# Kernel optimization log

Hardware: AMD Instinct MI355X
Metric: run time of the kernel (lower is better)

## Reference

```python
import jax, jax.numpy as jnp
import numpy as np


def setup_inputs() -> dict:
    key = jax.random.key(0)
    ks = jax.random.split(key, 8)
    B, De, Do, T, H, W = 4, 128, 512, 4, 30, 52
    s = 0.05  # weight init scale
    return {
        "m_in": jax.random.normal(ks[0], (B, De, T, H, W), jnp.float32),
        "m_out": jax.random.normal(ks[1], (B, Do, T, H, W), jnp.float32),
        "q_in": jax.random.normal(ks[2], (B, De, H, W), jnp.float32),
        "q_out": jax.random.normal(ks[3], (B, Do, H, W), jnp.float32),
        "wr": jax.random.normal(ks[4], (Do, 2 * Do), jnp.float32) * s,
        "br": jnp.zeros((Do,), jnp.float32),
        "wu": jax.random.normal(ks[5], (Do, 2 * Do), jnp.float32) * s,
        "bu": jnp.zeros((Do,), jnp.float32),
        "wc": jax.random.normal(ks[6], (Do, 2 * Do), jnp.float32) * s,
        "bc": jnp.zeros((Do,), jnp.float32),
    }


def reference(m_in, m_out, q_in, q_out, wr, br, wu, bu, wc, bc):
    B, De, T, H, W = m_in.shape
    Do = m_out.shape[1]
    PROP_LAYERS = 5

    # --- memory read: pairwise frame attention (bmm + softmax + bmm) ---
    # keys: all T memory frames flattened; queries: current frame.
    mi = m_in.reshape(B, De, T * H * W)            # [B, De, THW]
    qi = q_in.reshape(B, De, H * W)                # [B, De, HW]
    p = jnp.einsum('bdk,bdq->bkq', mi, qi) / (De ** 0.5)  # [B, THW, HW]
    p = jax.nn.softmax(p, axis=1)                  # softmax over memory locations (dim=1 in torch)
    mem = jnp.einsum('bok,bkq->boq', m_out.reshape(B, Do, T * H * W), p)
    mem = mem.reshape(B, Do, H, W)                 # mem_mean; identical every propagate layer

    # --- ConvGRU_h (kernel_size=1 => per-pixel linear gates) ---
    def conv1x1(w, b, x):
        return jnp.einsum('oc,bchw->bohw', w, x) + b[None, :, None, None]

    def gru(x, h):
        xh = jnp.concatenate([x, h], axis=1)                       # [B, 2*Do, H, W]
        r = jax.nn.sigmoid(conv1x1(wr, br, xh))
        u = jax.nn.sigmoid(conv1x1(wu, bu, xh))
        c = jnp.tanh(conv1x1(wc, bc, jnp.concatenate([x, r * h], axis=1)))
        return h * (1.0 - u) + u * c

    q0 = q_out
    q = q_out
    for _ in range(PROP_LAYERS):
        q = gru(q, mem)  # original: q_out = ConvGRU_h(q_out, mem_mean)
    return jnp.concatenate([q, q0], axis=1)  # [B, 2*Do, H, W]
```

## Files before the change

### kernel.cpp

```cpp
#include <hip/hip_runtime.h>
#include <hip/hip_bf16.h>
#include <math.h>

typedef unsigned short u16;
typedef __attribute__((ext_vector_type(8))) short bf16x8;
typedef __attribute__((ext_vector_type(4))) float f32x4;

__device__ __forceinline__ u16 f2bf(float f) {
  union { float f; unsigned u; } x; x.f = f;
  unsigned r = x.u + 0x7fffu + ((x.u >> 16) & 1u);
  return (u16)(r >> 16);
}
__device__ __forceinline__ float bf2f(u16 h) {
  union { unsigned u; float f; } x; x.u = ((unsigned)h) << 16;
  return x.f;
}
__device__ __forceinline__ float sigmf(float x) {
  x = fminf(fmaxf(x, -30.f), 30.f);
  return 1.f / (1.f + __expf(-x));
}
__device__ __forceinline__ float tanh_fast(float x) {
  x = fminf(fmaxf(x, -15.f), 15.f);
  float t = __expf(2.f * x);
  return (t - 1.f) / (t + 1.f);
}

template<int N> __device__ __forceinline__ void wait_vmcnt() {
  if constexpr (N == 0)      asm volatile("s_waitcnt vmcnt(0)" ::: "memory");
  else if constexpr (N == 4) asm volatile("s_waitcnt vmcnt(4)" ::: "memory");
  else if constexpr (N == 6) asm volatile("s_waitcnt vmcnt(6)" ::: "memory");
  else if constexpr (N == 9) asm volatile("s_waitcnt vmcnt(9)" ::: "memory");
  else static_assert(N == 0 || N == 4 || N == 6 || N == 9, "add vmcnt case");
}

#define NB 4
#define DE 128
#define DO_ 512
#define HW 1560
#define THW 6240
#define NP 1664
#define KP 6272
#define PROP 5
#define PVSPLIT 7
#define PVKC 896

template<int MODE, int BMT, int BKT>
__device__ __forceinline__
void gemm_core(const u16* __restrict__ A, const u16* __restrict__ Bt,
               int K, int lda, int ldb, long a_bs, long b_bs,
               void* __restrict__ out0v, long o0_bs, int ld0,
               u16* __restrict__ out1, long o1_bs, int ld1,
               const void* __restrict__ e0v, long e0_bs,
               const void* __restrict__ e1v, long e1_bs,
               const void* __restrict__ e2v, long e2_bs,
               int nvalid, float scale)
{
  constexpr int WR = BMT / 64;
  constexpr int WC = 4 / WR;
  constexpr int NF = 8 / WC;
  constexpr int KK = BKT / 32;
  constexpr int ASLOT = BMT * BKT / 8;
  constexpr int BSLOT = 128 * BKT / 8;
  constexpr int NISS = (ASLOT + BSLOT) / 256;
  constexpr int RSH = (BMT == 128) ? 7 : 6;
  __shared__ u16 lds[2][ASLOT + BSLOT][8];

  const int tid = threadIdx.x;
  const int wave = tid >> 6, lane = tid & 63;
  const int kg = lane >> 4, lr = lane & 15;
  const int wrw = wave / WC, wcw = wave % WC;
  const long b = blockIdx.z;
  const int m0 = blockIdx.x * BMT, n0 = blockIdx.y * 128;
  A += b * a_bs; Bt += b * b_bs;

  float* out0f = (float*)out0v;
  u16* out0h = (u16*)out0v;
  const float* e0f = (const float*)e0v;
  const u16* e0h = (const u16*)e0v;
  const u16* e1h = (const u16*)e1v;
  const u16* e2h = (const u16*)e2v;

  auto stage = [&](int buf, int kt) {
#pragma unroll
    for (int i = 0; i < NISS; ++i) {
      int s = tid + 256 * i;
      const u16* src;
      if (s < ASLOT) {
        int row = s & (BMT - 1), g = s >> RSH;
        src = A + (long)(m0 + row) * lda + kt + g * 8;
      } else {
        int s2 = s - ASLOT;
        int row = s2 & 127, g = s2 >> 7;
        src = Bt + (long)(n0 + row) * ldb + kt + g * 8;
      }
      __builtin_amdgcn_global_load_lds(
          (const __attribute__((address_space(1))) void*)src,
          (__attribute__((address_space(3))) void*)&lds[buf][wave * 64 + 256 * i][0],
          16, 0, 0);
    }
  };

  f32x4 acc[4][NF];
#pragma unroll
  for (int m = 0; m < 4; ++m)
#pragma unroll
    for (int n = 0; n < NF; ++n) acc[m][n] = (f32x4){0.f, 0.f, 0.f, 0.f};

  const int nt = K / BKT;
  stage(0, 0);
  for (int t = 0; t < nt; ++t) {
    int cur = t & 1;
    if (t + 1 < nt) {
      stage(cur ^ 1, (t + 1) * BKT);
      wait_vmcnt<NISS>();
    } else {
      wait_vmcnt<0>();
    }
    __builtin_amdgcn_s_barrier();
    bf16x8 af[KK][4], bfr[KK][NF];
#pragma unroll
    for (int kk = 0; kk < KK; ++kk) {
#pragma unroll
      for (int m = 0; m < 4; ++m)
        af[kk][m] = *(const bf16x8*)&lds[cur][(kk * 4 + kg) * BMT + wrw * 64 + m * 16 + lr][0];
#pragma unroll
      for (int n = 0; n < NF; ++n)
        bfr[kk][n] = *(const bf16x8*)&lds[cur][ASLOT + (kk * 4 + kg) * 128 + (wcw * NF + n) * 16 + lr][0];
    }
#pragma unroll
    for (int kk = 0; kk < KK; ++kk)
#pragma unroll
      for (int m = 0; m < 4; ++m)
#pragma unroll
        for (int n = 0; n < NF; ++n)
          acc[m][n] = __builtin_amdgcn_mfma_f32_16x16x32_bf16(af[kk][m], bfr[kk][n], acc[m][n], 0, 0, 0);
    __builtin_amdgcn_s_barrier();
  }

  if constexpr (MODE == 0) {
    float rs[4][4];
#pragma unroll
    for (int m = 0; m < 4; ++m)
#pragma unroll
      for (int j = 0; j < 4; ++j) rs[m][j] = 0.f;
#pragma unroll
    for (int m = 0; m < 4; ++m) {
      int rloc = wrw * 64 + m * 16 + kg * 4;
#pragma unroll
      for (int n = 0; n < NF; ++n) {
        int col = n0 + (wcw * NF + n) * 16 + lr;
#pragma unroll
        for (int j = 0; j < 4; ++j) {
          long row = m0 + rloc + j;
          float p = __expf(acc[m][n][j] * scale);
          bool valid = (col < nvalid);
          out1[b * o1_bs + row * ld1 + col] = valid ? f2bf(p) : (u16)0;
          rs[m][j] += valid ? p : 0.f;
        }
      }
    }
#pragma unroll
    for (int m = 0; m < 4; ++m)
#pragma unroll
      for (int j = 0; j < 4; ++j) {
#pragma unroll
        for (int msk = 1; msk < 16; msk <<= 1)
          rs[m][j] += __shfl_xor(rs[m][j], msk, 64);
      }
    float* zbuf = (float*)lds;
    if (lr == 0) {
#pragma unroll
      for (int m = 0; m < 4; ++m)
#pragma unroll
        for (int j = 0; j < 4; ++j)
          zbuf[wcw * 128 + wrw * 64 + m * 16 + kg * 4 + j] = rs[m][j];
    }
    __syncthreads();
    if (tid < 128)
      out0f[b * o0_bs + (long)blockIdx.y * NP + (m0 + tid)] = zbuf[tid] + zbuf[128 + tid];
    return;
  }

#pragma unroll
  for (int m = 0; m < 4; ++m) {
    int rloc = wrw * 64 + m * 16 + kg * 4;
#pragma unroll
    for (int n = 0; n < NF; ++n) {
      int col = n0 + (wcw * NF + n) * 16 + lr;
#pragma unroll
      for (int j = 0; j < 4; ++j) {
        long row = m0 + rloc + j;
        float v = acc[m][n][j];
        if constexpr (MODE == 2) {
          out1[b * o1_bs + row * ld1 + col] = f2bf(v + e0f[col]);
        } else if constexpr (MODE == 3) {
          float gt = sigmf(v + bf2f(e0h[b * e0_bs + row * 1024 + col]));
          if (col < 512)
            out1[b * o1_bs + row * ld1 + 512 + col] =
                f2bf(gt * bf2f(e1h[b * e1_bs + row * 512 + col]));
          else
            out0h[b * o0_bs + row * ld0 + (col - 512)] = f2bf(gt);
        } else if constexpr (MODE == 4) {
          float cg = tanh_fast(v + e0f[col]);
          float u = bf2f(e1h[b * e1_bs + row * 512 + col]);
          float mm = bf2f(e2h[b * e2_bs + row * 512 + col]);
          float x = mm * (1.f - u) + u * cg;
          out1[b * o1_bs + row * ld1 + col] = f2bf(x);
          if (out0f) out0f[b * o0_bs + row * ld0 + col] = x;
        }
      }
    }
  }
}

#define GEMM_ARGS                                                              \
  const u16* __restrict__ A, const u16* __restrict__ Bt, int K, int lda,       \
  int ldb, long a_bs, long b_bs, void* __restrict__ out0v, long o0_bs,         \
  int ld0, u16* __restrict__ out1, long o1_bs, int ld1,                        \
  const void* __restrict__ e0v, long e0_bs, const void* __restrict__ e1v,      \
  long e1_bs, const void* __restrict__ e2v, long e2_bs, int nvalid, float scale
#define GEMM_PASS A, Bt, K, lda, ldb, a_bs, b_bs, out0v, o0_bs, ld0, out1,     \
  o1_bs, ld1, e0v, e0_bs, e1v, e1_bs, e2v, e2_bs, nvalid, scale

__global__ __launch_bounds__(256) void gk_scores(GEMM_ARGS) { gemm_core<0, 128, 32>(GEMM_PASS); }
__global__ __launch_bounds__(256) void gk_chru(GEMM_ARGS)   { gemm_core<2, 64, 64>(GEMM_PASS); }
__global__ __launch_bounds__(256) void gk_gates(GEMM_ARGS)  { gemm_core<3, 64, 64>(GEMM_PASS); }
__global__ __launch_bounds__(256) void gk_cand(GEMM_ARGS)   { gemm_core<4, 64, 64>(GEMM_PASS); }

__global__ __launch_bounds__(256)
void gemm_pv(const u16* __restrict__ Pt, const u16* __restrict__ moutb,
             u16* __restrict__ Ppart)
{
  const int bid = blockIdx.x;
  const int xcd = bid & 7, i = bid >> 3;
  const int s = xcd * 91 + i;
  const int pair = s / 26, mb = s - pair * 26;
  const int b = pair / PVSPLIT, z = pair - b * PVSPLIT;
  const int m0 = mb * 64;
  const int k0 = z * PVKC;

  const u16* A = Pt + (long)b * NP * KP;
  const u16* B0;
  {
    const u16* Bb = moutb + (long)b * DO_ * KP;
    B0 = Bb + (long)((threadIdx.x >> 6) * 128 + (threadIdx.x & 15)) * KP +
         ((threadIdx.x & 63) >> 4) * 8;
  }

  __shared__ u16 lds[2][2048];
  const int tid = threadIdx.x;
  const int wave = tid >> 6, lane = tid & 63;
  const int kg = lane >> 4, lr = lane & 15;

  auto stage = [&](int buf, int kt) {
    int row = tid & 63, g = tid >> 6;
    const u16* src = A + (long)(m0 + row) * KP + kt + g * 8;
    __builtin_amdgcn_global_load_lds(
        (const __attribute__((address_space(1))) void*)src,
        (__attribute__((address_space(3))) void*)&lds[buf][(wave * 64) * 8],
        16, 0, 0);
  };

  f32x4 acc[4][8];
#pragma unroll
  for (int m = 0; m < 4; ++m)
#pragma unroll
    for (int n = 0; n < 8; ++n) acc[m][n] = (f32x4){0.f, 0.f, 0.f, 0.f};

  bf16x8 bra[8], brb[8];
#pragma unroll
  for (int n = 0; n < 8; ++n)
    bra[n] = *(const bf16x8*)&B0[(long)n * 16 * KP + k0];
  stage(0, k0);

#define PV_STEP(BU, BL, T, CUR)                                                  \
  {                                                                              \
    if ((T) + 1 < 28) {                                                          \
      int ktn = k0 + ((T) + 1) * 32;                                             \
      _Pragma("unroll") for (int n = 0; n < 8; ++n)                              \
          BL[n] = *(const bf16x8*)&B0[(long)n * 16 * KP + ktn];                  \
      stage((CUR) ^ 1, ktn);                                                     \
      wait_vmcnt<9>();                                                           \
    } else {                                                                     \
      wait_vmcnt<0>();                                                           \
    }                                                                            \
    __builtin_amdgcn_s_barrier();                                                \
    bf16x8 af[4];                                                                \
    _Pragma("unroll") for (int m = 0; m < 4; ++m)                                \
        af[m] = *(const bf16x8*)&lds[CUR][(kg * 64 + m * 16 + lr) * 8];          \
    _Pragma("unroll") for (int m = 0; m < 4; ++m)                                \
        _Pragma("unroll") for (int n = 0; n < 8; ++n)                            \
            acc[m][n] = __builtin_amdgcn_mfma_f32_16x16x32_bf16(af[m], BU[n],    \
                                                                acc[m][n], 0, 0, 0); \
    __builtin_amdgcn_s_barrier();                                                \
  }

  for (int tp = 0; tp < 14; ++tp) {
    PV_STEP(bra, brb, 2 * tp, 0);
    PV_STEP(brb, bra, 2 * tp + 1, 1);
  }
#undef PV_STEP

  u16* out = Ppart + (long)(b * PVSPLIT + z) * NP * DO_;
#pragma unroll
  for (int m = 0; m < 4; ++m) {
#pragma unroll
    for (int n = 0; n < 8; ++n) {
      int col = wave * 128 + n * 16 + lr;
#pragma unroll
      for (int j = 0; j < 4; ++j) {
        int row = m0 + m * 16 + kg * 4 + j;
        out[(long)row * DO_ + col] = f2bf(acc[m][n][j]);
      }
    }
  }
}

__global__ void k_transpose_cast(const float* __restrict__ in, u16* __restrict__ out,
                                 int R, int C, int Cp, int out_ld,
                                 long in_bs, long out_bs) {
  __shared__ float t[32][33];
  long b = blockIdx.z;
  int c0 = blockIdx.x * 32, r0 = blockIdx.y * 32;
  int tx = threadIdx.x, ty = threadIdx.y;
#pragma unroll
  for (int i = 0; i < 32; i += 8) {
    int r = r0 + ty + i, c = c0 + tx;
    t[ty + i][tx] = (r < R && c < C) ? in[b * in_bs + (long)r * C + c] : 0.f;
  }
  __syncthreads();
#pragma unroll
  for (int i = 0; i < 32; i += 8) {
    int c = c0 + ty + i, r = r0 + tx;
    if (c < Cp && r < R)
      out[b * out_bs + (long)c * out_ld + r] = f2bf(t[tx][ty + i]);
  }
}

__global__ void k_cast_pad(const float* __restrict__ in, u16* __restrict__ out,
                           int Cin, int Cout, long in_bs, long out_bs) {
  int c = blockIdx.x * 256 + threadIdx.x;
  int r = blockIdx.y;
  long b = blockIdx.z;
  if (c >= Cout) return;
  out[b * out_bs + (long)r * Cout + c] =
      (c < Cin) ? f2bf(in[b * in_bs + (long)r * Cin + c]) : (u16)0;
}

__global__ void k_build_wru(const float* __restrict__ wr_, const float* __restrict__ wu_,
                            u16* __restrict__ wrux, u16* __restrict__ wruh) {
  int k = blockIdx.x * 256 + threadIdx.x;
  int m = blockIdx.y;
  if (k >= 512) return;
  const float* src = (m < 512) ? wr_ : wu_;
  int mm = m & 511;
  wrux[m * 512 + k] = f2bf(src[mm * 1024 + k]);
  wruh[m * 512 + k] = f2bf(src[mm * 1024 + 512 + k]);
}

__global__ void k_bias_ru(const float* __restrict__ br_, const float* __restrict__ bu_,
                          float* __restrict__ bias) {
  int i = blockIdx.x * 256 + threadIdx.x;
  if (i < 1024) bias[i] = (i < 512) ? br_[i] : bu_[i - 512];
}

__global__ void k_invz(const float* __restrict__ Zp, float* __restrict__ invZ) {
  int t = blockIdx.x * 256 + threadIdx.x;
  if (t >= NB * NP) return;
  int b = t / NP, q = t - b * NP;
  const float* base = Zp + (long)b * 49 * NP + q;
  float s = 0.f;
#pragma unroll
  for (int nb = 0; nb < 49; ++nb) s += base[(long)nb * NP];
  invZ[t] = 1.f / s;
}

__global__ void k_reduce_mem(const u16* __restrict__ Ppart, const float* __restrict__ invZ,
                             u16* __restrict__ memTb) {
  long t = (long)blockIdx.x * 256 + threadIdx.x;
  const long bs = (long)NP * DO_;
  if (t >= (long)NB * bs / 8) return;
  long flat = t * 8;
  int b = (int)(flat / bs);
  long r = flat - (long)b * bs;
  int q = (int)(r / DO_);
  float s[8];
#pragma unroll
  for (int e = 0; e < 8; ++e) s[e] = 0.f;
#pragma unroll
  for (int z = 0; z < PVSPLIT; ++z) {
    uint4 v = *(const uint4*)&Ppart[(long)(b * PVSPLIT + z) * bs + r];
    s[0] += bf2f((u16)(v.x & 0xffff)); s[1] += bf2f((u16)(v.x >> 16));
    s[2] += bf2f((u16)(v.y & 0xffff)); s[3] += bf2f((u16)(v.y >> 16));
    s[4] += bf2f((u16)(v.z & 0xffff)); s[5] += bf2f((u16)(v.z >> 16));
    s[6] += bf2f((u16)(v.w & 0xffff)); s[7] += bf2f((u16)(v.w >> 16));
  }
  float iz = invZ[b * NP + q];
  uint4 o;
  o.x = (unsigned)f2bf(s[0] * iz) | ((unsigned)f2bf(s[1] * iz) << 16);
  o.y = (unsigned)f2bf(s[2] * iz) | ((unsigned)f2bf(s[3] * iz) << 16);
  o.z = (unsigned)f2bf(s[4] * iz) | ((unsigned)f2bf(s[5] * iz) << 16);
  o.w = (unsigned)f2bf(s[6] * iz) | ((unsigned)f2bf(s[7] * iz) << 16);
  *(uint4*)&memTb[(long)b * bs + r] = o;
}

__global__ void k_out_q(const float* __restrict__ Qfin, float* __restrict__ dout) {
  __shared__ float t[32][33];
  long b = blockIdx.z;
  int q0 = blockIdx.x * 32, ch0 = blockIdx.y * 32;
  int tx = threadIdx.x, ty = threadIdx.y;
#pragma unroll
  for (int i = 0; i < 32; i += 8)
    t[ty + i][tx] = Qfin[b * ((long)NP * 512) + (long)(q0 + ty + i) * 512 + ch0 + tx];
  __syncthreads();
#pragma unroll
  for (int i = 0; i < 32; i += 8) {
    int ch = ch0 + ty + i, q = q0 + tx;
    if (q < HW)
      dout[b * ((long)1024 * HW) + (long)ch * HW + q] = t[tx][ty + i];
  }
}

__global__ void k_copy_q0(const float4* __restrict__ src, float4* __restrict__ dst) {
  int idx = blockIdx.x * 256 + threadIdx.x;
  long b = blockIdx.z;
  const long n4 = (long)DO_ * HW / 4;
  if (idx < n4)
    dst[b * ((long)1024 * HW / 4) + n4 + idx] = src[b * n4 + idx];
}

extern "C" void kernel_launch(void* const* d_in, const int* in_sizes, int n_in,
                              void* d_out, int out_size, void* d_ws, size_t ws_size,
                              hipStream_t stream) {
  const float* m_in  = (const float*)d_in[0];
  const float* m_out = (const float*)d_in[1];
  const float* q_in  = (const float*)d_in[2];
  const float* q_out = (const float*)d_in[3];
  const float* wr    = (const float*)d_in[4];
  const float* br    = (const float*)d_in[5];
  const float* wu    = (const float*)d_in[6];
  const float* bu    = (const float*)d_in[7];
  const float* wc    = (const float*)d_in[8];
  const float* bc    = (const float*)d_in[9];
  float* dout = (float*)d_out;

  char* p = (char*)d_ws;
  size_t off = 0;
  auto alloc = [&](size_t bytes) { void* r = p + off; off += (bytes + 255) & ~(size_t)255; return r; };
  u16*   miT    = (u16*)alloc((size_t)NB * KP * DE * 2);
  u16*   qiT    = (u16*)alloc((size_t)NB * NP * DE * 2);
  u16*   Pt     = (u16*)alloc((size_t)NB * NP * KP * 2);
  float* invZ   = (float*)alloc((size_t)NB * NP * 4);
  u16*   moutb  = (u16*)alloc((size_t)NB * DO_ * KP * 2);
  u16*   memTb  = (u16*)alloc((size_t)NB * NP * DO_ * 2);
  u16*   chru   = (u16*)alloc((size_t)NB * NP * 1024 * 2);
  u16*   U      = (u16*)alloc((size_t)NB * NP * DO_ * 2);
  u16*   XRb    = (u16*)alloc((size_t)NB * NP * 1024 * 2);
  float* Qfin   = (float*)alloc((size_t)NB * NP * DO_ * 4);
  u16*   XRa    = (u16*)alloc((size_t)NB * NP * 1024 * 2);
  u16*   wrux   = (u16*)alloc((size_t)1024 * 512 * 2);
  u16*   wruh   = (u16*)alloc((size_t)1024 * 512 * 2);
  u16*   wcb    = (u16*)alloc((size_t)512 * 1024 * 2);
  float* biasru = (float*)alloc((size_t)1024 * 4);
  u16*   Ppart  = (u16*)chru;
  float* Zp     = (float*)memTb;
  if (off > ws_size) return;

  k_build_wru<<<dim3(2, 1024), 256, 0, stream>>>(wr, wu, wrux, wruh);
  k_cast_pad<<<dim3(4, 512, 1), 256, 0, stream>>>(wc, wcb, 1024, 1024, 0, 0);
  k_bias_ru<<<dim3(4), 256, 0, stream>>>(br, bu, biasru);
  k_cast_pad<<<dim3(25, 512, NB), 256, 0, stream>>>(
      m_out, moutb, THW, KP, (long)DO_ * THW, (long)DO_ * KP);
  k_transpose_cast<<<dim3(196, 4, NB), dim3(32, 8), 0, stream>>>(
      m_in, miT, DE, THW, KP, DE, (long)DE * THW, (long)KP * DE);
  k_transpose_cast<<<dim3(52, 4, NB), dim3(32, 8), 0, stream>>>(
      q_in, qiT, DE, HW, NP, DE, (long)DE * HW, (long)NP * DE);
  k_transpose_cast<<<dim3(52, 16, NB), dim3(32, 8), 0, stream>>>(
      q_out, XRa, DO_, HW, NP, 1024, (long)DO_ * HW, (long)NP * 1024);

  gk_scores<<<dim3(13, 49, NB), 256, 0, stream>>>(
      qiT, miT, DE, DE, DE, (long)NP * DE, (long)KP * DE,
      Zp, (long)49 * NP, 0, Pt, (long)NP * KP, KP,
      nullptr, 0, nullptr, 0, nullptr, 0, THW, 0.08838834764831845f);
  k_invz<<<dim3(26), 256, 0, stream>>>(Zp, invZ);

  gemm_pv<<<dim3(728), 256, 0, stream>>>(Pt, moutb, Ppart);
  k_reduce_mem<<<dim3(1664), 256, 0, stream>>>(Ppart, invZ, memTb);

  gk_chru<<<dim3(26, 8, NB), 256, 0, stream>>>(
      memTb, wruh, DO_, DO_, DO_, (long)NP * DO_, 0,
      nullptr, 0, 0, chru, (long)NP * 1024, 1024,
      biasru, 0, nullptr, 0, nullptr, 0, 0, 0.f);

  u16* xr[2] = {XRa, XRb};
  for (int l = 0; l < PROP; ++l) {
    u16* cur = xr[l & 1];
    u16* nxt = xr[(l + 1) & 1];
    gk_gates<<<dim3(26, 8, NB), 256, 0, stream>>>(
        cur, wrux, DO_, 1024, DO_, (long)NP * 1024, 0,
        U, (long)NP * DO_, DO_, cur, (long)NP * 1024, 1024,
        chru, (long)NP * 1024, memTb, (long)NP * DO_, nullptr, 0, 0, 0.f);
    gk_cand<<<dim3(26, 4, NB), 256, 0, stream>>>(
        cur, wcb, 1024, 1024, 1024, (long)NP * 1024, 0,
        (l == PROP - 1) ? (void*)Qfin : nullptr, (long)NP * DO_, DO_,
        nxt, (long)NP * 1024, 1024,
        bc, 0, U, (long)NP * DO_, memTb, (long)NP * DO_, 0, 0.f);
  }

  k_out_q<<<dim3(49, 16, NB), dim3(32, 8), 0, stream>>>(Qfin, dout);
  k_copy_q0<<<dim3(780, 1, NB), 256, 0, stream>>>((const float4*)q_out, (float4*)dout);
}
```

Baseline: 680.7 us.

## Fold candidate x-projection into gates GEMM and halve candidate GEMM K

The gates GEMM now also computes the Wc·x part of the candidate (N grows from 1024 to 1536) and writes it to a new Cx buffer, sharing the A-operand loads of x. The candidate GEMM then only multiplies r*h by the h-half of Wc (K 1024 to 512) and adds Cx in its epilogue, cutting a redundant re-read of x and K-loop work. Separately, gemm_pv replaces its manual vmcnt waits and raw barriers with __syncthreads and gets a 2-blocks-per-CU launch bound, which may lose the prefetch/compute overlap. Weight building is merged into one kernel.

```diff
diff --git a/kernel.cpp b/kernel.cpp
--- a/kernel.cpp
+++ b/kernel.cpp
@@ -29,8 +29,7 @@
   if constexpr (N == 0)      asm volatile("s_waitcnt vmcnt(0)" ::: "memory");
   else if constexpr (N == 4) asm volatile("s_waitcnt vmcnt(4)" ::: "memory");
   else if constexpr (N == 6) asm volatile("s_waitcnt vmcnt(6)" ::: "memory");
-  else if constexpr (N == 9) asm volatile("s_waitcnt vmcnt(9)" ::: "memory");
-  else static_assert(N == 0 || N == 4 || N == 6 || N == 9, "add vmcnt case");
+  else static_assert(N == 0 || N == 4 || N == 6, "add vmcnt case");
 }
 
 #define NB 4
@@ -50,9 +49,11 @@
                int K, int lda, int ldb, long a_bs, long b_bs,
                void* __restrict__ out0v, long o0_bs, int ld0,
                u16* __restrict__ out1, long o1_bs, int ld1,
+               u16* __restrict__ out2, long o2_bs,
                const void* __restrict__ e0v, long e0_bs,
                const void* __restrict__ e1v, long e1_bs,
                const void* __restrict__ e2v, long e2_bs,
+               const void* __restrict__ e3v, long e3_bs,
                int nvalid, float scale)
 {
   constexpr int WR = BMT / 64;
@@ -79,6 +80,7 @@
   const u16* e0h = (const u16*)e0v;
   const u16* e1h = (const u16*)e1v;
   const u16* e2h = (const u16*)e2v;
+  const u16* e3h = (const u16*)e3v;
 
   auto stage = [&](int buf, int kt) {
 #pragma unroll
@@ -194,14 +196,18 @@
         if constexpr (MODE == 2) {
           out1[b * o1_bs + row * ld1 + col] = f2bf(v + e0f[col]);
         } else if constexpr (MODE == 3) {
-          float gt = sigmf(v + bf2f(e0h[b * e0_bs + row * 1024 + col]));
-          if (col < 512)
-            out1[b * o1_bs + row * ld1 + 512 + col] =
-                f2bf(gt * bf2f(e1h[b * e1_bs + row * 512 + col]));
-          else
-            out0h[b * o0_bs + row * ld0 + (col - 512)] = f2bf(gt);
+          if (col < 1024) {
+            float gt = sigmf(v + bf2f(e0h[b * e0_bs + row * 1024 + col]));
+            if (col < 512)
+              out1[b * o1_bs + row * ld1 + 512 + col] =
+                  f2bf(gt * bf2f(e1h[b * e1_bs + row * 512 + col]));
+            else
+              out0h[b * o0_bs + row * ld0 + (col - 512)] = f2bf(gt);
+          } else {
+            out2[b * o2_bs + row * 512 + (col - 1024)] = f2bf(v);
+          }
         } else if constexpr (MODE == 4) {
-          float cg = tanh_fast(v + e0f[col]);
+          float cg = tanh_fast(v + bf2f(e3h[b * e3_bs + row * 512 + col]) + e0f[col]);
           float u = bf2f(e1h[b * e1_bs + row * 512 + col]);
           float mm = bf2f(e2h[b * e2_bs + row * 512 + col]);
           float x = mm * (1.f - u) + u * cg;
@@ -217,17 +223,20 @@
   const u16* __restrict__ A, const u16* __restrict__ Bt, int K, int lda,       \
   int ldb, long a_bs, long b_bs, void* __restrict__ out0v, long o0_bs,         \
   int ld0, u16* __restrict__ out1, long o1_bs, int ld1,                        \
+  u16* __restrict__ out2, long o2_bs,                                          \
   const void* __restrict__ e0v, long e0_bs, const void* __restrict__ e1v,      \
-  long e1_bs, const void* __restrict__ e2v, long e2_bs, int nvalid, float scale
+  long e1_bs, const void* __restrict__ e2v, long e2_bs,                        \
+  const void* __restrict__ e3v, long e3_bs, int nvalid, float scale
 #define GEMM_PASS A, Bt, K, lda, ldb, a_bs, b_bs, out0v, o0_bs, ld0, out1,     \
-  o1_bs, ld1, e0v, e0_bs, e1v, e1_bs, e2v, e2_bs, nvalid, scale
+  o1_bs, ld1, out2, o2_bs, e0v, e0_bs, e1v, e1_bs, e2v, e2_bs, e3v, e3_bs,     \
+  nvalid, scale
 
 __global__ __launch_bounds__(256) void gk_scores(GEMM_ARGS) { gemm_core<0, 128, 32>(GEMM_PASS); }
 __global__ __launch_bounds__(256) void gk_chru(GEMM_ARGS)   { gemm_core<2, 64, 64>(GEMM_PASS); }
 __global__ __launch_bounds__(256) void gk_gates(GEMM_ARGS)  { gemm_core<3, 64, 64>(GEMM_PASS); }
 __global__ __launch_bounds__(256) void gk_cand(GEMM_ARGS)   { gemm_core<4, 64, 64>(GEMM_PASS); }
 
-__global__ __launch_bounds__(256)
+__global__ __launch_bounds__(256, 2)
 void gemm_pv(const u16* __restrict__ Pt, const u16* __restrict__ moutb,
              u16* __restrict__ Ppart)
 {
@@ -272,6 +281,7 @@
   for (int n = 0; n < 8; ++n)
     bra[n] = *(const bf16x8*)&B0[(long)n * 16 * KP + k0];
   stage(0, k0);
+  __syncthreads();
 
 #define PV_STEP(BU, BL, T, CUR)                                                  \
   {                                                                              \
@@ -280,11 +290,7 @@
       _Pragma("unroll") for (int n = 0; n < 8; ++n)                              \
           BL[n] = *(const bf16x8*)&B0[(long)n * 16 * KP + ktn];                  \
       stage((CUR) ^ 1, ktn);                                                     \
-      wait_vmcnt<9>();                                                           \
-    } else {                                                                     \
-      wait_vmcnt<0>();                                                           \
     }                                                                            \
-    __builtin_amdgcn_s_barrier();                                                \
     bf16x8 af[4];                                                                \
     _Pragma("unroll") for (int m = 0; m < 4; ++m)                                \
         af[m] = *(const bf16x8*)&lds[CUR][(kg * 64 + m * 16 + lr) * 8];          \
@@ -292,7 +298,7 @@
         _Pragma("unroll") for (int n = 0; n < 8; ++n)                            \
             acc[m][n] = __builtin_amdgcn_mfma_f32_16x16x32_bf16(af[m], BU[n],    \
                                                                 acc[m][n], 0, 0, 0); \
-    __builtin_amdgcn_s_barrier();                                                \
+    __syncthreads();                                                             \
   }
 
   for (int tp = 0; tp < 14; ++tp) {
@@ -347,15 +353,24 @@
       (c < Cin) ? f2bf(in[b * in_bs + (long)r * Cin + c]) : (u16)0;
 }
 
-__global__ void k_build_wru(const float* __restrict__ wr_, const float* __restrict__ wu_,
-                            u16* __restrict__ wrux, u16* __restrict__ wruh) {
+__global__ void k_build_w(const float* __restrict__ wr_, const float* __restrict__ wu_,
+                          const float* __restrict__ wc_,
+                          u16* __restrict__ wruh, u16* __restrict__ wruxc,
+                          u16* __restrict__ wch) {
   int k = blockIdx.x * 256 + threadIdx.x;
   int m = blockIdx.y;
   if (k >= 512) return;
-  const float* src = (m < 512) ? wr_ : wu_;
-  int mm = m & 511;
-  wrux[m * 512 + k] = f2bf(src[mm * 1024 + k]);
-  wruh[m * 512 + k] = f2bf(src[mm * 1024 + 512 + k]);
+  if (m < 1024) {
+    const float* src = (m < 512) ? wr_ : wu_;
+    wruh[m * 512 + k] = f2bf(src[(m & 511) * 1024 + 512 + k]);
+  } else if (m < 2560) {
+    int n = m - 1024;
+    const float* src = (n < 512) ? wr_ : ((n < 1024) ? wu_ : wc_);
+    wruxc[n * 512 + k] = f2bf(src[(n & 511) * 1024 + k]);
+  } else {
+    int n = m - 2560;
+    wch[n * 512 + k] = f2bf(wc_[n * 1024 + 512 + k]);
+  }
 }
 
 __global__ void k_bias_ru(const float* __restrict__ br_, const float* __restrict__ bu_,
@@ -458,16 +473,16 @@
   u16*   XRb    = (u16*)alloc((size_t)NB * NP * 1024 * 2);
   float* Qfin   = (float*)alloc((size_t)NB * NP * DO_ * 4);
   u16*   XRa    = (u16*)alloc((size_t)NB * NP * 1024 * 2);
-  u16*   wrux   = (u16*)alloc((size_t)1024 * 512 * 2);
+  u16*   Cx     = (u16*)alloc((size_t)NB * NP * 512 * 2);
   u16*   wruh   = (u16*)alloc((size_t)1024 * 512 * 2);
-  u16*   wcb    = (u16*)alloc((size_t)512 * 1024 * 2);
+  u16*   wruxc  = (u16*)alloc((size_t)1536 * 512 * 2);
+  u16*   wch    = (u16*)alloc((size_t)512 * 512 * 2);
   float* biasru = (float*)alloc((size_t)1024 * 4);
   u16*   Ppart  = (u16*)chru;
   float* Zp     = (float*)memTb;
   if (off > ws_size) return;
 
-  k_build_wru<<<dim3(2, 1024), 256, 0, stream>>>(wr, wu, wrux, wruh);
-  k_cast_pad<<<dim3(4, 512, 1), 256, 0, stream>>>(wc, wcb, 1024, 1024, 0, 0);
+  k_build_w<<<dim3(2, 3072), 256, 0, stream>>>(wr, wu, wc, wruh, wruxc, wch);
   k_bias_ru<<<dim3(4), 256, 0, stream>>>(br, bu, biasru);
   k_cast_pad<<<dim3(25, 512, NB), 256, 0, stream>>>(
       m_out, moutb, THW, KP, (long)DO_ * THW, (long)DO_ * KP);
@@ -480,8 +495,8 @@
 
   gk_scores<<<dim3(13, 49, NB), 256, 0, stream>>>(
       qiT, miT, DE, DE, DE, (long)NP * DE, (long)KP * DE,
-      Zp, (long)49 * NP, 0, Pt, (long)NP * KP, KP,
-      nullptr, 0, nullptr, 0, nullptr, 0, THW, 0.08838834764831845f);
+      Zp, (long)49 * NP, 0, Pt, (long)NP * KP, KP, nullptr, 0,
+      nullptr, 0, nullptr, 0, nullptr, 0, nullptr, 0, THW, 0.08838834764831845f);
   k_invz<<<dim3(26), 256, 0, stream>>>(Zp, invZ);
 
   gemm_pv<<<dim3(728), 256, 0, stream>>>(Pt, moutb, Ppart);
@@ -489,22 +504,25 @@
 
   gk_chru<<<dim3(26, 8, NB), 256, 0, stream>>>(
       memTb, wruh, DO_, DO_, DO_, (long)NP * DO_, 0,
-      nullptr, 0, 0, chru, (long)NP * 1024, 1024,
-      biasru, 0, nullptr, 0, nullptr, 0, 0, 0.f);
+      nullptr, 0, 0, chru, (long)NP * 1024, 1024, nullptr, 0,
+      biasru, 0, nullptr, 0, nullptr, 0, nullptr, 0, 0, 0.f);
 
   u16* xr[2] = {XRa, XRb};
   for (int l = 0; l < PROP; ++l) {
     u16* cur = xr[l & 1];
     u16* nxt = xr[(l + 1) & 1];
-    gk_gates<<<dim3(26, 8, NB), 256, 0, stream>>>(
-        cur, wrux, DO_, 1024, DO_, (long)NP * 1024, 0,
+    gk_gates<<<dim3(26, 12, NB), 256, 0, stream>>>(
+        cur, wruxc, DO_, 1024, DO_, (long)NP * 1024, 0,
         U, (long)NP * DO_, DO_, cur, (long)NP * 1024, 1024,
-        chru, (long)NP * 1024, memTb, (long)NP * DO_, nullptr, 0, 0, 0.f);
+        Cx, (long)NP * 512,
+        chru, (long)NP * 1024, memTb, (long)NP * DO_, nullptr, 0,
+        nullptr, 0, 0, 0.f);
     gk_cand<<<dim3(26, 4, NB), 256, 0, stream>>>(
-        cur, wcb, 1024, 1024, 1024, (long)NP * 1024, 0,
+        cur + 512, wch, DO_, 1024, DO_, (long)NP * 1024, 0,
         (l == PROP - 1) ? (void*)Qfin : nullptr, (long)NP * DO_, DO_,
-        nxt, (long)NP * 1024, 1024,
-        bc, 0, U, (long)NP * DO_, memTb, (long)NP * DO_, 0, 0.f);
+        nxt, (long)NP * 1024, 1024, nullptr, 0,
+        bc, 0, U, (long)NP * DO_, memTb, (long)NP * DO_,
+        Cx, (long)NP * 512, 0, 0.f);
   }
 
   k_out_q<<<dim3(49, 16, NB), dim3(32, 8), 0, stream>>>(Qfin, dout);
```

Result: faster. 656.7 us (-3.5%).
